# Kernel optimization log

Hardware: AMD Instinct MI355X
Metric: run time of the kernel (lower is better)

The kernel has to match this reference:

```python
import jax, jax.numpy as jnp
import numpy as np

B = 4096       # batch_size
D = 128        # projection dim
TEMP = 0.5     # temperature
EPS = 1e-12    # F.normalize eps


def setup_inputs() -> dict:
    key = jax.random.key(0)
    k1, k2 = jax.random.split(key)
    zi = jax.random.normal(k1, (B, D), dtype=jnp.float32)
    zj = jax.random.normal(k2, (B, D), dtype=jnp.float32)
    return {"zi": zi, "zj": zj}


def _l2_normalize(x):
    n = jnp.sqrt(jnp.sum(x * x, axis=-1, keepdims=True))
    return x / jnp.maximum(n, EPS)


def reference(zi, zj):
    zi_n = _l2_normalize(zi)
    zj_n = _l2_normalize(zj)

    # four [B, B] similarity matrices
    lii = jnp.matmul(zi_n, zi_n.T) / TEMP
    lij = jnp.matmul(zi_n, zj_n.T) / TEMP
    lji = jnp.matmul(zj_n, zi_n.T) / TEMP
    ljj = jnp.matmul(zj_n, zj_n.T) / TEMP

    # positives: diagonal of ij and ji (row-major gather of ~mask == diagonal)
    pos = jnp.concatenate([jnp.diagonal(lij), jnp.diagonal(lji)], axis=0)[:, None]  # [2B, 1]

    # off-diagonal gather: for row r, columns != r (preserves row-major order of mask gather)
    r = jnp.arange(B)[:, None]          # [B, 1]
    c = jnp.arange(B - 1)[None, :]      # [1, B-1]
    cols = c + (c >= r).astype(c.dtype)  # [B, B-1]

    def offdiag(m):
        return jnp.take_along_axis(m, cols, axis=1)  # [B, B-1]

    neg_i = jnp.concatenate([offdiag(lii), offdiag(lij)], axis=1)  # [B, 2B-2]
    neg_j = jnp.concatenate([offdiag(lji), offdiag(ljj)], axis=1)  # [B, 2B-2]
    neg = jnp.concatenate([neg_i, neg_j], axis=0)                  # [2B, 2B-2]

    logits = jnp.concatenate([pos, neg], axis=1)                   # [2B, 2B-1]

    # cross-entropy with all labels == 0
    loss = jnp.mean(jax.nn.logsumexp(logits, axis=1) - logits[:, 0])
    return loss
```

## Files before the change

kernel.cpp:

```cpp
#include <hip/hip_runtime.h>
#include <hip/hip_bf16.h>

#define BATCH   4096
#define TWO_B   8192
#define DIM     128
#define INV_TEMP 2.0f
#define SFOLD 1.6986436f

typedef __attribute__((ext_vector_type(8))) short bf16x8;
typedef __attribute__((ext_vector_type(4))) float f32x4;

#define NTB 32
#define NPAIRS (NTB * (NTB + 1) / 2)

#define ZB_BYTES   (TWO_B * DIM * 2)
#define RS_OFFSET  ZB_BYTES
#define PS_OFFSET  (RS_OFFSET + TWO_B * 4)

__global__ __launch_bounds__(256) void k_normalize(const float* __restrict__ zi,
                                                   const float* __restrict__ zj,
                                                   __hip_bfloat16* __restrict__ zb,
                                                   float* __restrict__ ps,
                                                   float* __restrict__ rowsum) {
    int w = threadIdx.x >> 6;
    int lane = threadIdx.x & 63;
    int r = blockIdx.x * 4 + w;

    if (threadIdx.x < 8) rowsum[blockIdx.x * 8 + threadIdx.x] = 0.0f;

    float2 vi = *reinterpret_cast<const float2*>(zi + (size_t)r * DIM + lane * 2);
    float2 vj = *reinterpret_cast<const float2*>(zj + (size_t)r * DIM + lane * 2);
    float ssi = vi.x * vi.x + vi.y * vi.y;
    float ssj = vj.x * vj.x + vj.y * vj.y;
    #pragma unroll
    for (int m = 1; m < 64; m <<= 1) {
        ssi += __shfl_xor(ssi, m, 64);
        ssj += __shfl_xor(ssj, m, 64);
    }
    float invi = 1.0f / fmaxf(sqrtf(ssi), 1e-12f);
    float invj = 1.0f / fmaxf(sqrtf(ssj), 1e-12f);

    float nix = vi.x * invi, niy = vi.y * invi;
    float njx = vj.x * invj, njy = vj.y * invj;

    __hip_bfloat162 hi2, hj2;
    hi2.x = __float2bfloat16(nix * SFOLD);
    hi2.y = __float2bfloat16(niy * SFOLD);
    hj2.x = __float2bfloat16(njx * SFOLD);
    hj2.y = __float2bfloat16(njy * SFOLD);
    *reinterpret_cast<__hip_bfloat162*>(zb + (size_t)r * DIM + lane * 2) = hi2;
    *reinterpret_cast<__hip_bfloat162*>(zb + (size_t)(r + BATCH) * DIM + lane * 2) = hj2;

    float d = nix * njx + niy * njy;
    #pragma unroll
    for (int m = 1; m < 64; m <<= 1) d += __shfl_xor(d, m, 64);

    __shared__ float red[4];
    if (lane == 0) red[w] = d;
    __syncthreads();
    if (threadIdx.x == 0)
        ps[blockIdx.x] = red[0] + red[1] + red[2] + red[3];
}

__global__ __launch_bounds__(256, 2) void k_sim(const __hip_bfloat16* __restrict__ zb,
                                                float* __restrict__ rowsum) {
    __shared__ float colacc[128];

    const int t = threadIdx.x;
    const int w = t >> 6;
    const int lane = t & 63;
    const int lo = lane & 15, hi = lane >> 4;

    const int pair = blockIdx.x >> 1;
    const int cs   = blockIdx.x & 1;
    int rb = 0, accum = 0;
    while (accum + (NTB - rb) <= pair) { accum += NTB - rb; ++rb; }
    const int cb = rb + (pair - accum);
    const bool offdiag = (rb != cb);

    const int rowBase = rb * 256 + w * 64;
    const int colWin  = cb * 256 + cs * 128;

    if (t < 128) colacc[t] = 0.0f;
    __syncthreads();

    const char* zbB = reinterpret_cast<const char*>(zb);

    bf16x8 a[4][4];
    #pragma unroll
    for (int i = 0; i < 4; ++i) {
        const char* rp = zbB + (size_t)(rowBase + i * 16 + lo) * 256 + hi * 16;
        #pragma unroll
        for (int ks = 0; ks < 4; ++ks)
            a[i][ks] = *reinterpret_cast<const bf16x8*>(rp + ks * 64);
    }

    float psum[4][4];
    #pragma unroll
    for (int i = 0; i < 4; ++i)
        #pragma unroll
        for (int p = 0; p < 4; ++p) psum[i][p] = 0.0f;

    #pragma unroll
    for (int ct = 0; ct < 2; ++ct) {
        const int colBase = colWin + ct * 64;

        bf16x8 b[4][4];
        #pragma unroll
        for (int j = 0; j < 4; ++j) {
            const char* rp = zbB + (size_t)(colBase + j * 16 + lo) * 256 + hi * 16;
            #pragma unroll
            for (int ks = 0; ks < 4; ++ks)
                b[j][ks] = *reinterpret_cast<const bf16x8*>(rp + ks * 64);
        }

        f32x4 acc[4][4];
        #pragma unroll
        for (int i = 0; i < 4; ++i)
            #pragma unroll
            for (int j = 0; j < 4; ++j) acc[i][j] = (f32x4){0.f, 0.f, 0.f, 0.f};

        #pragma unroll
        for (int ks = 0; ks < 4; ++ks)
            #pragma unroll
            for (int i = 0; i < 4; ++i)
                #pragma unroll
                for (int j = 0; j < 4; ++j)
                    acc[i][j] = __builtin_amdgcn_mfma_f32_16x16x32_bf16(
                        a[i][ks], b[j][ks], acc[i][j], 0, 0, 0);

        float cps[4] = {0.f, 0.f, 0.f, 0.f};
        const bool diagTile = (colBase == rowBase);
        #pragma unroll
        for (int i = 0; i < 4; ++i) {
            #pragma unroll
            for (int p = 0; p < 4; ++p) {
                float s = 0.0f;
                #pragma unroll
                for (int j = 0; j < 4; ++j) {
                    float e = exp2f(acc[i][j][p]);
                    if (diagTile && j == i && lo == hi * 4 + p) e = 0.0f;
                    s += e;
                    cps[j] += e;
                }
                psum[i][p] += s;
            }
        }

        if (offdiag) {
            #pragma unroll
            for (int j = 0; j < 4; ++j) {
                float v = cps[j];
                v += __shfl_xor(v, 16, 64);
                v += __shfl_xor(v, 32, 64);
                if (hi == 0)
                    atomicAdd(&colacc[ct * 64 + j * 16 + lo], v);
            }
        }
    }

    #pragma unroll
    for (int i = 0; i < 4; ++i) {
        #pragma unroll
        for (int p = 0; p < 4; ++p) {
            float s = psum[i][p];
            s += __shfl_xor(s, 1, 64);
            s += __shfl_xor(s, 2, 64);
            s += __shfl_xor(s, 4, 64);
            s += __shfl_xor(s, 8, 64);
            if (lo == 0)
                atomicAdd(&rowsum[rowBase + i * 16 + hi * 4 + p], s);
        }
    }

    if (offdiag) {
        __syncthreads();
        if (t < 128) atomicAdd(&rowsum[colWin + t], colacc[t]);
    }
}

__global__ __launch_bounds__(1024) void k_final(const float* __restrict__ rowsum,
                                                const float* __restrict__ ps,
                                                float* __restrict__ out) {
    __shared__ float redl[1024];
    __shared__ float redp[1024];
    const int t = threadIdx.x;

    float s = 0.0f;
    #pragma unroll
    for (int q = 0; q < TWO_B / 1024; ++q) s += logf(rowsum[t + q * 1024]);
    float p = ps[t];

    redl[t] = s;
    redp[t] = p;
    __syncthreads();
    #pragma unroll
    for (int off = 512; off > 0; off >>= 1) {
        if (t < off) {
            redl[t] += redl[t + off];
            redp[t] += redp[t + off];
        }
        __syncthreads();
    }
    if (t == 0)
        out[0] = (redl[0] - 2.0f * INV_TEMP * redp[0]) / (float)TWO_B;
}

extern "C" void kernel_launch(void* const* d_in, const int* in_sizes, int n_in,
                              void* d_out, int out_size, void* d_ws, size_t ws_size,
                              hipStream_t stream) {
    const float* zi = (const float*)d_in[0];
    const float* zj = (const float*)d_in[1];
    float* out = (float*)d_out;

    char* ws = (char*)d_ws;
    __hip_bfloat16* zb = (__hip_bfloat16*)ws;
    float* rowsum = (float*)(ws + RS_OFFSET);
    float* ps = (float*)(ws + PS_OFFSET);

    k_normalize<<<BATCH / 4, 256, 0, stream>>>(zi, zj, zb, ps, rowsum);
    k_sim<<<NPAIRS * 2, 256, 0, stream>>>(zb, rowsum);
    k_final<<<1, 1024, 0, stream>>>(rowsum, ps, out);
}
```

Measured before the change: 55.36 us.

## Stage 128x128 tiles in swizzled LDS via direct global-to-LDS loads

```diff
diff --git a/kernel.cpp b/kernel.cpp
--- a/kernel.cpp
+++ b/kernel.cpp
@@ -10,12 +10,18 @@
 typedef __attribute__((ext_vector_type(8))) short bf16x8;
 typedef __attribute__((ext_vector_type(4))) float f32x4;
 
-#define NTB 32
-#define NPAIRS (NTB * (NTB + 1) / 2)
+#define NT 64
+#define NPAIRS (NT * (NT + 1) / 2)
 
 #define ZB_BYTES   (TWO_B * DIM * 2)
 #define RS_OFFSET  ZB_BYTES
 #define PS_OFFSET  (RS_OFFSET + TWO_B * 4)
+
+__device__ __forceinline__ void gload16(const void* g, void* l) {
+    __builtin_amdgcn_global_load_lds(
+        (const __attribute__((address_space(1))) unsigned int*)g,
+        (__attribute__((address_space(3))) unsigned int*)l, 16, 0, 0);
+}
 
 __global__ __launch_bounds__(256) void k_normalize(const float* __restrict__ zi,
                                                    const float* __restrict__ zj,
@@ -64,98 +70,98 @@
 
 __global__ __launch_bounds__(256, 2) void k_sim(const __hip_bfloat16* __restrict__ zb,
                                                 float* __restrict__ rowsum) {
+    __shared__ unsigned short As[128 * 128];
+    __shared__ unsigned short Bs[128 * 128];
     __shared__ float colacc[128];
 
     const int t = threadIdx.x;
     const int w = t >> 6;
     const int lane = t & 63;
     const int lo = lane & 15, hi = lane >> 4;
-
-    const int pair = blockIdx.x >> 1;
-    const int cs   = blockIdx.x & 1;
+    const int wr = w >> 1, wc = w & 1;
+
+    const int pair = blockIdx.x;
     int rb = 0, accum = 0;
-    while (accum + (NTB - rb) <= pair) { accum += NTB - rb; ++rb; }
+    while (accum + (NT - rb) <= pair) { accum += NT - rb; ++rb; }
     const int cb = rb + (pair - accum);
     const bool offdiag = (rb != cb);
 
-    const int rowBase = rb * 256 + w * 64;
-    const int colWin  = cb * 256 + cs * 128;
+    const int rbase = rb * 128;
+    const int cbase = cb * 128;
 
     if (t < 128) colacc[t] = 0.0f;
+
+    const char* zbB = reinterpret_cast<const char*>(zb);
+    char* AsB = reinterpret_cast<char*>(As);
+    char* BsB = reinterpret_cast<char*>(Bs);
+
+    #pragma unroll
+    for (int it = 0; it < 8; ++it) {
+        int chunk = it * 256 + w * 64;
+        int c = chunk + lane;
+        int row = c >> 4, blk = c & 15;
+        const char* srcA = zbB + (size_t)(rbase + row) * 256 + ((blk ^ (row & 7)) * 16);
+        gload16(srcA, AsB + chunk * 16);
+    }
+    if (offdiag) {
+        #pragma unroll
+        for (int it = 0; it < 8; ++it) {
+            int chunk = it * 256 + w * 64;
+            int c = chunk + lane;
+            int row = c >> 4, blk = c & 15;
+            const char* srcB = zbB + (size_t)(cbase + row) * 256 + ((blk ^ (row & 7)) * 16);
+            gload16(srcB, BsB + chunk * 16);
+        }
+    }
     __syncthreads();
 
-    const char* zbB = reinterpret_cast<const char*>(zb);
-
-    bf16x8 a[4][4];
-    #pragma unroll
-    for (int i = 0; i < 4; ++i) {
-        const char* rp = zbB + (size_t)(rowBase + i * 16 + lo) * 256 + hi * 16;
-        #pragma unroll
-        for (int ks = 0; ks < 4; ++ks)
-            a[i][ks] = *reinterpret_cast<const bf16x8*>(rp + ks * 64);
-    }
-
-    float psum[4][4];
+    const char* AsC = reinterpret_cast<const char*>(As);
+    const char* BsC = offdiag ? reinterpret_cast<const char*>(Bs) : AsC;
+
+    f32x4 acc[4][4];
     #pragma unroll
     for (int i = 0; i < 4; ++i)
         #pragma unroll
-        for (int p = 0; p < 4; ++p) psum[i][p] = 0.0f;
-
-    #pragma unroll
-    for (int ct = 0; ct < 2; ++ct) {
-        const int colBase = colWin + ct * 64;
-
-        bf16x8 b[4][4];
+        for (int j = 0; j < 4; ++j) acc[i][j] = (f32x4){0.f, 0.f, 0.f, 0.f};
+
+    #pragma unroll
+    for (int ks = 0; ks < 4; ++ks) {
+        bf16x8 a[4], b[4];
+        #pragma unroll
+        for (int i = 0; i < 4; ++i) {
+            int r = wr * 64 + i * 16 + lo;
+            int bk = (ks * 4 + hi) ^ (r & 7);
+            a[i] = *reinterpret_cast<const bf16x8*>(AsC + r * 256 + bk * 16);
+        }
         #pragma unroll
         for (int j = 0; j < 4; ++j) {
-            const char* rp = zbB + (size_t)(colBase + j * 16 + lo) * 256 + hi * 16;
-            #pragma unroll
-            for (int ks = 0; ks < 4; ++ks)
-                b[j][ks] = *reinterpret_cast<const bf16x8*>(rp + ks * 64);
-        }
-
-        f32x4 acc[4][4];
+            int r = wc * 64 + j * 16 + lo;
+            int bk = (ks * 4 + hi) ^ (r & 7);
+            b[j] = *reinterpret_cast<const bf16x8*>(BsC + r * 256 + bk * 16);
+        }
         #pragma unroll
         for (int i = 0; i < 4; ++i)
             #pragma unroll
-            for (int j = 0; j < 4; ++j) acc[i][j] = (f32x4){0.f, 0.f, 0.f, 0.f};
-
-        #pragma unroll
-        for (int ks = 0; ks < 4; ++ks)
-            #pragma unroll
-            for (int i = 0; i < 4; ++i)
-                #pragma unroll
-                for (int j = 0; j < 4; ++j)
-                    acc[i][j] = __builtin_amdgcn_mfma_f32_16x16x32_bf16(
-                        a[i][ks], b[j][ks], acc[i][j], 0, 0, 0);
-
-        float cps[4] = {0.f, 0.f, 0.f, 0.f};
-        const bool diagTile = (colBase == rowBase);
-        #pragma unroll
-        for (int i = 0; i < 4; ++i) {
-            #pragma unroll
-            for (int p = 0; p < 4; ++p) {
-                float s = 0.0f;
-                #pragma unroll
-                for (int j = 0; j < 4; ++j) {
-                    float e = exp2f(acc[i][j][p]);
-                    if (diagTile && j == i && lo == hi * 4 + p) e = 0.0f;
-                    s += e;
-                    cps[j] += e;
-                }
-                psum[i][p] += s;
-            }
-        }
-
-        if (offdiag) {
+            for (int j = 0; j < 4; ++j)
+                acc[i][j] = __builtin_amdgcn_mfma_f32_16x16x32_bf16(
+                    a[i], b[j], acc[i][j], 0, 0, 0);
+    }
+
+    float psum[4][4];
+    float cps[4] = {0.f, 0.f, 0.f, 0.f};
+    #pragma unroll
+    for (int i = 0; i < 4; ++i) {
+        #pragma unroll
+        for (int p = 0; p < 4; ++p) {
+            float s = 0.0f;
             #pragma unroll
             for (int j = 0; j < 4; ++j) {
-                float v = cps[j];
-                v += __shfl_xor(v, 16, 64);
-                v += __shfl_xor(v, 32, 64);
-                if (hi == 0)
-                    atomicAdd(&colacc[ct * 64 + j * 16 + lo], v);
+                float e = exp2f(acc[i][j][p]);
+                if (!offdiag && wr == wc && j == i && lo == hi * 4 + p) e = 0.0f;
+                s += e;
+                cps[j] += e;
             }
+            psum[i][p] = s;
         }
     }
 
@@ -169,13 +175,21 @@
             s += __shfl_xor(s, 4, 64);
             s += __shfl_xor(s, 8, 64);
             if (lo == 0)
-                atomicAdd(&rowsum[rowBase + i * 16 + hi * 4 + p], s);
+                atomicAdd(&rowsum[rbase + wr * 64 + i * 16 + hi * 4 + p], s);
         }
     }
 
     if (offdiag) {
+        #pragma unroll
+        for (int j = 0; j < 4; ++j) {
+            float v = cps[j];
+            v += __shfl_xor(v, 16, 64);
+            v += __shfl_xor(v, 32, 64);
+            if (hi == 0)
+                atomicAdd(&colacc[wc * 64 + j * 16 + lo], v);
+        }
         __syncthreads();
-        if (t < 128) atomicAdd(&rowsum[colWin + t], colacc[t]);
+        if (t < 128) atomicAdd(&rowsum[cbase + t], colacc[t]);
     }
 }
 
@@ -219,6 +233,6 @@
     float* ps = (float*)(ws + PS_OFFSET);
 
     k_normalize<<<BATCH / 4, 256, 0, stream>>>(zi, zj, zb, ps, rowsum);
-    k_sim<<<NPAIRS * 2, 256, 0, stream>>>(zb, rowsum);
+    k_sim<<<NPAIRS, 256, 0, stream>>>(zb, rowsum);
     k_final<<<1, 1024, 0, stream>>>(rowsum, ps, out);
 }
```

Result: slower. 59.02 us (+6.6%).
